# Kernel optimization log

Measured on AMD Instinct MI355X. Metric: run time of the kernel, lower is better.

Reference implementation:

```python
import jax, jax.numpy as jnp
import numpy as np
from jax import lax

D_MODEL = 1024
D_IN = 1024        # expand=1 -> d_inner = d_model
N_STATE = 16       # d_state
DT_RANK = 64       # ceil(d_model/16)
D_FFN = 4096
BATCH, SEQ = 2, 2048


def setup_inputs() -> dict:
    key = jax.random.key(0)
    ks = jax.random.split(key, 12)
    r = lambda i, shape, s=0.02: jax.random.normal(ks[i], shape, jnp.float32) * s
    ones = lambda n: jnp.ones((n,), jnp.float32)
    zeros = lambda n: jnp.zeros((n,), jnp.float32)
    # S4D-real init for A
    A_log = jnp.log(jnp.tile(jnp.arange(1, N_STATE + 1, dtype=jnp.float32), (D_IN, 1)))
    return {
        "src": jax.random.normal(ks[0], (BATCH, SEQ, D_MODEL), jnp.float32),
        "in_proj_w": r(1, (2 * D_IN, D_MODEL)),
        "conv_w": r(2, (D_IN, 2), 0.5),
        "conv_b": zeros(D_IN),
        "x_proj_w": r(3, (DT_RANK + 2 * N_STATE, D_IN)),
        "dt_proj_w": r(4, (D_IN, DT_RANK), 0.1),
        "dt_proj_b": r(5, (D_IN,), 0.1),
        "A_log": A_log,
        "Dp": ones(D_IN),
        "out_proj_w": r(6, (D_MODEL, D_IN)),
        "mnorm_g": ones(D_MODEL), "mnorm_b": zeros(D_MODEL),
        "n1_g": ones(D_MODEL), "n1_b": zeros(D_MODEL),
        "n2_g": ones(D_MODEL), "n2_b": zeros(D_MODEL),
        "n3_g": ones(D_MODEL), "n3_b": zeros(D_MODEL),
        "ffn_w1": r(7, (D_FFN, D_MODEL)),
        "ffn_w2": r(8, (D_MODEL, D_FFN)),
        "fe_w": r(9, (D_MODEL, D_MODEL)),
        "fe_b": zeros(D_MODEL),
    }


def _ln(x, g, b, eps=1e-5):
    m = x.mean(-1, keepdims=True)
    v = ((x - m) ** 2).mean(-1, keepdims=True)
    return (x - m) / jnp.sqrt(v + eps) * g + b


def _mamba(x, in_proj_w, conv_w, conv_b, x_proj_w, dt_proj_w, dt_proj_b,
           A_log, Dp, out_proj_w):
    B, L, _ = x.shape
    xz = x @ in_proj_w.T                       # (B,L,2*D_IN)
    x_in, z = jnp.split(xz, 2, axis=-1)
    # depthwise causal conv1d, kernel size 2: y[l] = w0*x[l-1] + w1*x[l] + b
    x_prev = jnp.pad(x_in, ((0, 0), (1, 0), (0, 0)))[:, :L]
    x_c = jax.nn.silu(x_prev * conv_w[:, 0] + x_in * conv_w[:, 1] + conv_b)
    x_dbl = x_c @ x_proj_w.T                   # (B,L,DT_RANK+2N)
    dt, Bm, Cm = jnp.split(x_dbl, [DT_RANK, DT_RANK + N_STATE], axis=-1)
    delta = jax.nn.softplus(dt @ dt_proj_w.T + dt_proj_b)   # (B,L,D_IN)
    A = -jnp.exp(A_log)                        # (D_IN,N)
    deltaA = jnp.exp(delta[..., None] * A)                   # (B,L,D_IN,N)
    dBu = delta[..., None] * Bm[:, :, None, :] * x_c[..., None]

    def step(h, t):
        dA_t, dBu_t, C_t = t                   # (B,D_IN,N),(B,D_IN,N),(B,N)
        h = dA_t * h + dBu_t
        y = jnp.einsum('bdn,bn->bd', h, C_t)
        return h, y

    h0 = jnp.zeros((B, D_IN, N_STATE), x.dtype)
    _, ys = lax.scan(step, h0,
                     (deltaA.transpose(1, 0, 2, 3),
                      dBu.transpose(1, 0, 2, 3),
                      Cm.transpose(1, 0, 2)))
    y = ys.transpose(1, 0, 2)                  # (B,L,D_IN)
    y = (y + x_c * Dp) * jax.nn.silu(z)
    return y @ out_proj_w.T


def reference(src, in_proj_w, conv_w, conv_b, x_proj_w, dt_proj_w, dt_proj_b,
              A_log, Dp, out_proj_w, mnorm_g, mnorm_b, n1_g, n1_b, n2_g, n2_b,
              n3_g, n3_b, ffn_w1, ffn_w2, fe_w, fe_b):
    # src1 = MambaBlock(norm1(src)); dropout = identity (eval)
    h = _mamba(_ln(src, n1_g, n1_b), in_proj_w, conv_w, conv_b, x_proj_w,
               dt_proj_w, dt_proj_b, A_log, Dp, out_proj_w)
    src = src + _ln(h, mnorm_g, mnorm_b)
    # FFN: Linear -> LeakyReLU(0.01) -> Linear (no bias)
    f = _ln(src, n2_g, n2_b) @ ffn_w1.T
    f = jnp.where(f >= 0, f, 0.01 * f) @ ffn_w2.T
    src = src + f
    src = src + (_ln(src, n3_g, n3_b) @ fe_w.T + fe_b)
    return src
```

## Files before the change

### kernel.cpp

```cpp
#include <hip/hip_runtime.h>
#include <hip/hip_bf16.h>
#include <cstddef>

#define L_SEQ   2048
#define NBATCH  2
#define NROWS   (NBATCH * L_SEQ)
#define NSTATE  16
#define CH      64
#define NCHUNK  (L_SEQ / CH)

typedef __bf16 bf16x8 __attribute__((ext_vector_type(8)));
typedef float  f32x4  __attribute__((ext_vector_type(4)));
typedef unsigned short u16x4 __attribute__((ext_vector_type(4)));
typedef unsigned short u16x8 __attribute__((ext_vector_type(8)));

static __device__ __forceinline__ unsigned short f2bf(float f) {
  unsigned int x = __builtin_bit_cast(unsigned int, f);
  x += 0x7fffu + ((x >> 16) & 1u);
  return (unsigned short)(x >> 16);
}
static __device__ __forceinline__ float bf2f(unsigned short u) {
  return __builtin_bit_cast(float, ((unsigned int)u) << 16);
}

#define GLDS(g, l) __builtin_amdgcn_global_load_lds( \
    (const __attribute__((address_space(1))) void*)(g), \
    (__attribute__((address_space(3))) void*)(l), 16, 0, 0)

#define DRAIN_VM() asm volatile("s_waitcnt vmcnt(0)" ::: "memory")

__global__ __launch_bounds__(256) void cvt_bf16_kernel(
    const float* __restrict__ in, unsigned short* __restrict__ out, int n4)
{
  const int i = blockIdx.x * 256 + threadIdx.x;
  if (i < n4) {
    const float4 v = reinterpret_cast<const float4*>(in)[i];
    u16x4 o;
    o[0] = f2bf(v.x); o[1] = f2bf(v.y); o[2] = f2bf(v.z); o[3] = f2bf(v.w);
    reinterpret_cast<u16x4*>(out)[i] = o;
  }
}

__global__ __launch_bounds__(256) void cvt_all_kernel(
    const float* __restrict__ ipw, const float* __restrict__ xpw,
    const float* __restrict__ dtw, const float* __restrict__ opw,
    const float* __restrict__ w1,  const float* __restrict__ w2,
    const float* __restrict__ few, float* __restrict__ zx,
    unsigned short* __restrict__ o_ipw, unsigned short* __restrict__ o_xpw,
    unsigned short* __restrict__ o_dtw, unsigned short* __restrict__ o_opw,
    unsigned short* __restrict__ o_w1,  unsigned short* __restrict__ o_w2,
    unsigned short* __restrict__ o_few,
    const float* __restrict__ lsrc, const float* __restrict__ lg,
    const float* __restrict__ lb, unsigned short* __restrict__ louth)
{
  __shared__ float sm[8];
  if (blockIdx.x >= 12832) {
    const int row = blockIdx.x - 12832;
    const int tid = threadIdx.x;
    const float4 v = reinterpret_cast<const float4*>(lsrc + (size_t)row * 1024)[tid];
    float s = v.x + v.y + v.z + v.w;
#pragma unroll
    for (int o = 32; o > 0; o >>= 1) s += __shfl_down(s, o, 64);
    if ((tid & 63) == 0) sm[tid >> 6] = s;
    __syncthreads();
    const float mean = (sm[0] + sm[1] + sm[2] + sm[3]) * (1.f / 1024.f);
    const float dx = v.x - mean, dy = v.y - mean, dz = v.z - mean, dw = v.w - mean;
    float q = dx * dx + dy * dy + dz * dz + dw * dw;
#pragma unroll
    for (int o = 32; o > 0; o >>= 1) q += __shfl_down(q, o, 64);
    __syncthreads();
    if ((tid & 63) == 0) sm[tid >> 6] = q;
    __syncthreads();
    const float var = (sm[0] + sm[1] + sm[2] + sm[3]) * (1.f / 1024.f);
    const float rstd = rsqrtf(var + 1e-5f);
    const float4 gv = reinterpret_cast<const float4*>(lg)[tid];
    const float4 bv = reinterpret_cast<const float4*>(lb)[tid];
    u16x4 ob;
    ob[0] = f2bf(dx * rstd * gv.x + bv.x);
    ob[1] = f2bf(dy * rstd * gv.y + bv.y);
    ob[2] = f2bf(dz * rstd * gv.z + bv.z);
    ob[3] = f2bf(dw * rstd * gv.w + bv.w);
    reinterpret_cast<u16x4*>(louth + (size_t)row * 1024)[tid] = ob;
    return;
  }
  int i = blockIdx.x * 256 + threadIdx.x;
  if (i < 98304) {
    reinterpret_cast<float4*>(zx)[i] = make_float4(0.f, 0.f, 0.f, 0.f);
    return;
  }
  i -= 98304;
  const float* src; unsigned short* dst;
  if (i < 524288)                 { src = ipw; dst = o_ipw; }
  else if ((i -= 524288) < 24576) { src = xpw; dst = o_xpw; }
  else if ((i -= 24576) < 16384)  { src = dtw; dst = o_dtw; }
  else if ((i -= 16384) < 262144) { src = opw; dst = o_opw; }
  else if ((i -= 262144) < 1048576){ src = w1; dst = o_w1; }
  else if ((i -= 1048576) < 1048576){ src = w2; dst = o_w2; }
  else if ((i -= 1048576) < 262144){ src = few; dst = o_few; }
  else return;
  const float4 v = reinterpret_cast<const float4*>(src)[i];
  u16x4 o;
  o[0] = f2bf(v.x); o[1] = f2bf(v.y); o[2] = f2bf(v.z); o[3] = f2bf(v.w);
  reinterpret_cast<u16x4*>(dst)[i] = o;
}

__global__ __launch_bounds__(256) void ln_kernel(
    const float* __restrict__ in, const float* __restrict__ g,
    const float* __restrict__ bta, const float* __restrict__ res,
    float* __restrict__ out, unsigned short* __restrict__ outb)
{
  const int row = blockIdx.x;
  const int tid = threadIdx.x;
  __shared__ float sm[8];
  const float4 v = reinterpret_cast<const float4*>(in + (size_t)row * 1024)[tid];
  float s = v.x + v.y + v.z + v.w;
#pragma unroll
  for (int o = 32; o > 0; o >>= 1) s += __shfl_down(s, o, 64);
  if ((tid & 63) == 0) sm[tid >> 6] = s;
  __syncthreads();
  const float mean = (sm[0] + sm[1] + sm[2] + sm[3]) * (1.f / 1024.f);
  const float dx = v.x - mean, dy = v.y - mean, dz = v.z - mean, dw = v.w - mean;
  float q = dx * dx + dy * dy + dz * dz + dw * dw;
#pragma unroll
  for (int o = 32; o > 0; o >>= 1) q += __shfl_down(q, o, 64);
  __syncthreads();
  if ((tid & 63) == 0) sm[tid >> 6] = q;
  __syncthreads();
  const float var = (sm[0] + sm[1] + sm[2] + sm[3]) * (1.f / 1024.f);
  const float rstd = rsqrtf(var + 1e-5f);
  const float4 gv = reinterpret_cast<const float4*>(g)[tid];
  const float4 bv = reinterpret_cast<const float4*>(bta)[tid];
  float4 o4;
  o4.x = dx * rstd * gv.x + bv.x;
  o4.y = dy * rstd * gv.y + bv.y;
  o4.z = dz * rstd * gv.z + bv.z;
  o4.w = dw * rstd * gv.w + bv.w;
  if (outb) {
    u16x4 ob;
    ob[0] = f2bf(o4.x); ob[1] = f2bf(o4.y); ob[2] = f2bf(o4.z); ob[3] = f2bf(o4.w);
    reinterpret_cast<u16x4*>(outb + (size_t)row * 1024)[tid] = ob;
  } else {
    if (res) {
      const float4 rv = reinterpret_cast<const float4*>(res + (size_t)row * 1024)[tid];
      o4.x += rv.x; o4.y += rv.y; o4.z += rv.z; o4.w += rv.w;
    }
    reinterpret_cast<float4*>(out + (size_t)row * 1024)[tid] = o4;
  }
}

__global__ __launch_bounds__(256) void ln2_kernel(
    const float* __restrict__ in, const float* __restrict__ g1,
    const float* __restrict__ b1, const float* __restrict__ res,
    const float* __restrict__ g2, const float* __restrict__ b2,
    float* __restrict__ out1, unsigned short* __restrict__ out2b)
{
  const int row = blockIdx.x;
  const int tid = threadIdx.x;
  __shared__ float sm[8];
  const float4 v = reinterpret_cast<const float4*>(in + (size_t)row * 1024)[tid];
  float s = v.x + v.y + v.z + v.w;
#pragma unroll
  for (int o = 32; o > 0; o >>= 1) s += __shfl_down(s, o, 64);
  if ((tid & 63) == 0) sm[tid >> 6] = s;
  __syncthreads();
  const float mean = (sm[0] + sm[1] + sm[2] + sm[3]) * (1.f / 1024.f);
  const float dx = v.x - mean, dy = v.y - mean, dz = v.z - mean, dw = v.w - mean;
  float q = dx * dx + dy * dy + dz * dz + dw * dw;
#pragma unroll
  for (int o = 32; o > 0; o >>= 1) q += __shfl_down(q, o, 64);
  __syncthreads();
  if ((tid & 63) == 0) sm[tid >> 6] = q;
  __syncthreads();
  const float var = (sm[0] + sm[1] + sm[2] + sm[3]) * (1.f / 1024.f);
  const float rstd = rsqrtf(var + 1e-5f);
  const float4 g1v = reinterpret_cast<const float4*>(g1)[tid];
  const float4 b1v = reinterpret_cast<const float4*>(b1)[tid];
  const float4 rv = reinterpret_cast<const float4*>(res + (size_t)row * 1024)[tid];
  float4 o4;
  o4.x = dx * rstd * g1v.x + b1v.x + rv.x;
  o4.y = dy * rstd * g1v.y + b1v.y + rv.y;
  o4.z = dz * rstd * g1v.z + b1v.z + rv.z;
  o4.w = dw * rstd * g1v.w + b1v.w + rv.w;
  reinterpret_cast<float4*>(out1 + (size_t)row * 1024)[tid] = o4;
  __syncthreads();
  float s2 = o4.x + o4.y + o4.z + o4.w;
#pragma unroll
  for (int o = 32; o > 0; o >>= 1) s2 += __shfl_down(s2, o, 64);
  if ((tid & 63) == 0) sm[tid >> 6] = s2;
  __syncthreads();
  const float mean2 = (sm[0] + sm[1] + sm[2] + sm[3]) * (1.f / 1024.f);
  const float ex = o4.x - mean2, ey = o4.y - mean2, ez = o4.z - mean2, ew = o4.w - mean2;
  float q2 = ex * ex + ey * ey + ez * ez + ew * ew;
#pragma unroll
  for (int o = 32; o > 0; o >>= 1) q2 += __shfl_down(q2, o, 64);
  __syncthreads();
  if ((tid & 63) == 0) sm[tid >> 6] = q2;
  __syncthreads();
  const float var2 = (sm[0] + sm[1] + sm[2] + sm[3]) * (1.f / 1024.f);
  const float rstd2 = rsqrtf(var2 + 1e-5f);
  const float4 g2v = reinterpret_cast<const float4*>(g2)[tid];
  const float4 b2v = reinterpret_cast<const float4*>(b2)[tid];
  u16x4 ob;
  ob[0] = f2bf(ex * rstd2 * g2v.x + b2v.x);
  ob[1] = f2bf(ey * rstd2 * g2v.y + b2v.y);
  ob[2] = f2bf(ez * rstd2 * g2v.z + b2v.z);
  ob[3] = f2bf(ew * rstd2 * g2v.w + b2v.w);
  reinterpret_cast<u16x4*>(out2b + (size_t)row * 1024)[tid] = ob;
}

__global__ __launch_bounds__(512) void gemm256_kernel(
    const unsigned short* __restrict__ A, int lda,
    const unsigned short* __restrict__ B, int ldb,
    void* __restrict__ Cv, int ldc,
    const float* __restrict__ bias, const float* __restrict__ res,
    int K, int act, int outbf, int gy)
{
  __shared__ __align__(16) unsigned char smem[131072];
  const int t = threadIdx.x;
  const int w = t >> 6, l = t & 63;

  const int q = gridDim.x >> 3;
  const int nid = (blockIdx.x & 7) * q + (blockIdx.x >> 3);
  const int bm = (nid / gy) * 256;
  const int bn = (nid % gy) * 256;

  const int wr = (w >> 2) * 128;
  const int wc = (w & 3) * 64;
  f32x4 acc[8][4] = {};

  const int srow = t >> 2;
  const int sk = (t & 3) * 8;
  const unsigned short* gA = A + (size_t)(bm + srow) * lda + sk;
  const unsigned short* gB = B + (size_t)(bn + srow) * ldb + sk;

  const int fr = l & 15;
  const int kb = (l >> 4) * 8;

#define SA7(s) (smem + (s) * 16384)
#define SB7(s) (smem + 65536 + (s) * 16384)

#define STAGE7(s, k0) do { \
    GLDS(gA + (k0), SA7(s) + w * 1024); \
    GLDS(gA + (k0) + (size_t)128 * lda, SA7(s) + 8192 + w * 1024); \
    GLDS(gB + (k0), SB7(s) + w * 1024); \
    GLDS(gB + (k0) + (size_t)128 * ldb, SB7(s) + 8192 + w * 1024); \
  } while (0)

#define COMPUTE7(s) do { \
    bf16x8 af[8], bfr[4]; \
    _Pragma("unroll") \
    for (int j = 0; j < 4; ++j) \
      bfr[j] = *reinterpret_cast<const bf16x8*>((const unsigned short*)SB7(s) + (wc + j * 16 + fr) * 32 + kb); \
    _Pragma("unroll") \
    for (int i = 0; i < 8; ++i) \
      af[i] = *reinterpret_cast<const bf16x8*>((const unsigned short*)SA7(s) + (wr + i * 16 + fr) * 32 + kb); \
    _Pragma("unroll") \
    for (int i = 0; i < 8; ++i) \
      _Pragma("unroll") \
      for (int j = 0; j < 4; ++j) \
        acc[i][j] = __builtin_amdgcn_mfma_f32_16x16x32_bf16(af[i], bfr[j], acc[i][j], 0, 0, 0); \
  } while (0)

  const int nt = K >> 5;
  STAGE7(0, 0);
  if (nt > 1) STAGE7(1, 32);
  if (nt > 2) STAGE7(2, 64);
  if (nt > 2)      asm volatile("s_waitcnt vmcnt(8)" ::: "memory");
  else if (nt > 1) asm volatile("s_waitcnt vmcnt(4)" ::: "memory");
  else             asm volatile("s_waitcnt vmcnt(0)" ::: "memory");
  __builtin_amdgcn_s_barrier();
  for (int kt = 0; kt < nt; ++kt) {
    const int s = kt & 3;
    __builtin_amdgcn_sched_barrier(0);
    if (kt + 3 < nt) STAGE7((kt + 3) & 3, (kt + 3) * 32);
    __builtin_amdgcn_sched_barrier(0);
    COMPUTE7(s);
    __builtin_amdgcn_sched_barrier(0);
    if (kt + 3 < nt)      asm volatile("s_waitcnt vmcnt(8)" ::: "memory");
    else if (kt + 2 < nt) asm volatile("s_waitcnt vmcnt(4)" ::: "memory");
    else if (kt + 1 < nt) asm volatile("s_waitcnt vmcnt(0)" ::: "memory");
    __builtin_amdgcn_s_barrier();
  }
#undef STAGE7
#undef COMPUTE7
#undef SA7
#undef SB7

  const int crow = (l >> 4) * 4;
  const int ccol = l & 15;
  float* Cf = (float*)Cv;
  unsigned short* Cb = (unsigned short*)Cv;
#pragma unroll
  for (int i = 0; i < 8; ++i) {
#pragma unroll
    for (int j = 0; j < 4; ++j) {
      const int n = bn + wc + j * 16 + ccol;
      const float bv = bias ? bias[n] : 0.f;
#pragma unroll
      for (int r = 0; r < 4; ++r) {
        const int m = bm + wr + i * 16 + crow + r;
        float v = acc[i][j][r] + bv;
        if (act == 1) v = (v > 20.f) ? v : __logf(1.f + __expf(v));
        else if (act == 2) v = (v >= 0.f) ? v : 0.01f * v;
        if (res) v += res[(size_t)m * ldc + n];
        if (outbf) Cb[(size_t)m * ldc + n] = f2bf(v);
        else       Cf[(size_t)m * ldc + n] = v;
      }
    }
  }
}

template<int BK>
__global__ __launch_bounds__(512) void gemm_ksplit_kernel(
    const unsigned short* __restrict__ A, int lda,
    const unsigned short* __restrict__ B, int ldb,
    void* __restrict__ Cv, int ldc,
    const float* __restrict__ bias, const float* __restrict__ res,
    int K, int act, int outbf, int gy)
{
  constexpr int ABYTES = 128 * BK * 2;
  constexpr int NISS = (BK == 32) ? 2 : 4;
  constexpr int RPI  = (BK == 32) ? 64 : 32;
  constexpr int NS   = BK / 32;
  __shared__ __align__(16) unsigned char smem[8 * ABYTES];
  const int tid = threadIdx.x;
  const int grp = tid >> 8;
  const int t = tid & 255;
  const int w = t >> 6, l = t & 63;

  const int q = gridDim.x >> 3;
  const int nid = (blockIdx.x & 7) * q + (blockIdx.x >> 3);
  const int bm = (nid / gy) * 128;
  const int bn = (nid % gy) * 128;

  const int K2 = K >> 1;
  const int koff = grp * K2;
  const int wr = (w >> 1) * 64, wc = (w & 1) * 64;
  f32x4 acc[4][4] = {};

  const int srow = (BK == 32) ? (t >> 2) : (t >> 3);
  const int sk   = (BK == 32) ? ((t & 3) * 8) : ((t & 7) * 8);
  const unsigned short* gA = A + (size_t)(bm + srow) * lda + koff + sk;
  const unsigned short* gB = B + (size_t)(bn + srow) * ldb + koff + sk;

  const int gbase = grp * 2 * ABYTES;
  const int fr = l & 15;
  const int kb = (l >> 4) * 8;

#define SAb(buf) (smem + gbase + (buf) * ABYTES)
#define SBb(buf) (smem + 4 * ABYTES + gbase + (buf) * ABYTES)

#define STAGEK(buf, k0) do { \
    _Pragma("unroll") \
    for (int ii = 0; ii < NISS; ++ii) { \
      GLDS(gA + (k0) + (size_t)ii * RPI * lda, SAb(buf) + ii * 4096 + w * 1024); \
      GLDS(gB + (k0) + (size_t)ii * RPI * ldb, SBb(buf) + ii * 4096 + w * 1024); \
    } \
  } while (0)

#define COMPUTEK(buf) do { \
    _Pragma("unroll") \
    for (int s = 0; s < NS; ++s) { \
      bf16x8 af[4], bfr[4]; \
      _Pragma("unroll") \
      for (int i = 0; i < 4; ++i) \
        af[i] = *reinterpret_cast<const bf16x8*>((const unsigned short*)SAb(buf) + (wr + i * 16 + fr) * BK + s * 32 + kb); \
      _Pragma("unroll") \
      for (int j = 0; j < 4; ++j) \
        bfr[j] = *reinterpret_cast<const bf16x8*>((const unsigned short*)SBb(buf) + (wc + j * 16 + fr) * BK + s * 32 + kb); \
      _Pragma("unroll") \
      for (int i = 0; i < 4; ++i) \
        _Pragma("unroll") \
        for (int j = 0; j < 4; ++j) \
          acc[i][j] = __builtin_amdgcn_mfma_f32_16x16x32_bf16(af[i], bfr[j], acc[i][j], 0, 0, 0); \
    } \
  } while (0)

  STAGEK(0, 0);
  DRAIN_VM();
  __syncthreads();
  int cur = 0;
  for (int k0 = BK; k0 < K2; k0 += BK) {
    __builtin_amdgcn_sched_barrier(0);
    STAGEK(cur ^ 1, k0);
    __builtin_amdgcn_sched_barrier(0);
    COMPUTEK(cur);
    DRAIN_VM();
    __syncthreads();
    cur ^= 1;
  }
  COMPUTEK(cur);
#undef STAGEK
#undef COMPUTEK
#undef SAb
#undef SBb

  __syncthreads();
  float* red = (float*)smem;
  if (grp) {
#pragma unroll
    for (int i = 0; i < 4; ++i)
#pragma unroll
      for (int j = 0; j < 4; ++j)
        *reinterpret_cast<f32x4*>(&red[(t << 6) + (i * 4 + j) * 4]) = acc[i][j];
  }
  __syncthreads();
  if (!grp) {
    const int crow = (l >> 4) * 4;
    const int ccol = l & 15;
    float* Cf = (float*)Cv;
    unsigned short* Cb = (unsigned short*)Cv;
#pragma unroll
    for (int i = 0; i < 4; ++i) {
#pragma unroll
      for (int j = 0; j < 4; ++j) {
        const f32x4 o = *reinterpret_cast<const f32x4*>(&red[(t << 6) + (i * 4 + j) * 4]);
        const int n = bn + wc + j * 16 + ccol;
        const float bv = bias ? bias[n] : 0.f;
#pragma unroll
        for (int r = 0; r < 4; ++r) {
          const int m = bm + wr + i * 16 + crow + r;
          float v = acc[i][j][r] + o[r] + bv;
          if (act == 1) v = (v > 20.f) ? v : __logf(1.f + __expf(v));
          else if (act == 2) v = (v >= 0.f) ? v : 0.01f * v;
          if (res) v += res[(size_t)m * ldc + n];
          if (outbf) Cb[(size_t)m * ldc + n] = f2bf(v);
          else       Cf[(size_t)m * ldc + n] = v;
        }
      }
    }
  }
}

__global__ __launch_bounds__(512) void gemm_ksplit_bn64_kernel(
    const unsigned short* __restrict__ A, int lda,
    const unsigned short* __restrict__ B, int ldb,
    void* __restrict__ Cv, int ldc,
    const float* __restrict__ bias, const float* __restrict__ res,
    int K, int act, int outbf, int gy)
{
  __shared__ __align__(16) unsigned char smem[49152];
  const int tid = threadIdx.x;
  const int grp = tid >> 8;
  const int t = tid & 255;
  const int w = t >> 6, l = t & 63;

  const int q = gridDim.x >> 3;
  const int nid = (blockIdx.x & 7) * q + (blockIdx.x >> 3);
  const int bm = (nid / gy) * 128;
  const int bn = (nid % gy) * 64;

  const int K2 = K >> 1;
  const int koff = grp * K2;
  const int wr = (w >> 1) * 64, wc = (w & 1) * 32;
  f32x4 acc[4][2] = {};

  const int srow = t >> 2;
  const int sk = (t & 3) * 8;
  const unsigned short* gA = A + (size_t)(bm + srow) * lda + koff + sk;
  const unsigned short* gB = B + (size_t)(bn + srow) * ldb + koff + sk;

  const int fr = l & 15;
  const int kb = (l >> 4) * 8;

#define SAn(buf) (smem + grp * 16384 + (buf) * 8192)
#define SBn(buf) (smem + 32768 + grp * 8192 + (buf) * 4096)

#define STAGEN(buf, k0) do { \
    GLDS(gA + (k0), SAn(buf) + w * 1024); \
    GLDS(gA + (k0) + (size_t)64 * lda, SAn(buf) + 4096 + w * 1024); \
    GLDS(gB + (k0), SBn(buf) + w * 1024); \
  } while (0)

#define COMPUTEN(buf) do { \
    bf16x8 af[4], bfr[2]; \
    _Pragma("unroll") \
    for (int i = 0; i < 4; ++i) \
      af[i] = *reinterpret_cast<const bf16x8*>((const unsigned short*)SAn(buf) + (wr + i * 16 + fr) * 32 + kb); \
    _Pragma("unroll") \
    for (int j = 0; j < 2; ++j) \
      bfr[j] = *reinterpret_cast<const bf16x8*>((const unsigned short*)SBn(buf) + (wc + j * 16 + fr) * 32 + kb); \
    _Pragma("unroll") \
    for (int i = 0; i < 4; ++i) \
      _Pragma("unroll") \
      for (int j = 0; j < 2; ++j) \
        acc[i][j] = __builtin_amdgcn_mfma_f32_16x16x32_bf16(af[i], bfr[j], acc[i][j], 0, 0, 0); \
  } while (0)

  STAGEN(0, 0);
  DRAIN_VM();
  __syncthreads();
  int cur = 0;
  for (int k0 = 32; k0 < K2; k0 += 32) {
    __builtin_amdgcn_sched_barrier(0);
    STAGEN(cur ^ 1, k0);
    __builtin_amdgcn_sched_barrier(0);
    COMPUTEN(cur);
    DRAIN_VM();
    __syncthreads();
    cur ^= 1;
  }
  COMPUTEN(cur);
#undef STAGEN
#undef COMPUTEN
#undef SAn
#undef SBn

  __syncthreads();
  float* red = (float*)smem;
  if (grp) {
#pragma unroll
    for (int i = 0; i < 4; ++i)
#pragma unroll
      for (int j = 0; j < 2; ++j)
        *reinterpret_cast<f32x4*>(&red[(t << 5) + (i * 2 + j) * 4]) = acc[i][j];
  }
  __syncthreads();
  if (!grp) {
    const int crow = (l >> 4) * 4;
    const int ccol = l & 15;
    float* Cf = (float*)Cv;
    unsigned short* Cb = (unsigned short*)Cv;
#pragma unroll
    for (int i = 0; i < 4; ++i) {
#pragma unroll
      for (int j = 0; j < 2; ++j) {
        const f32x4 o = *reinterpret_cast<const f32x4*>(&red[(t << 5) + (i * 2 + j) * 4]);
        const int n = bn + wc + j * 16 + ccol;
        const float bv = bias ? bias[n] : 0.f;
#pragma unroll
        for (int r = 0; r < 4; ++r) {
          const int m = bm + wr + i * 16 + crow + r;
          float v = acc[i][j][r] + o[r] + bv;
          if (act == 1) v = (v > 20.f) ? v : __logf(1.f + __expf(v));
          else if (act == 2) v = (v >= 0.f) ? v : 0.01f * v;
          if (res) v += res[(size_t)m * ldc + n];
          if (outbf) Cb[(size_t)m * ldc + n] = f2bf(v);
          else       Cf[(size_t)m * ldc + n] = v;
        }
      }
    }
  }
}

__global__ __launch_bounds__(512) void gemm_ksplit_ring_kernel(
    const unsigned short* __restrict__ A, int lda,
    const unsigned short* __restrict__ B, int ldb,
    void* __restrict__ Cv, int ldc,
    const float* __restrict__ bias, const float* __restrict__ res,
    int K, int act, int outbf, int gy)
{
  __shared__ __align__(16) unsigned char smem[131072];
  const int tid = threadIdx.x;
  const int grp = tid >> 8;
  const int t = tid & 255;
  const int w = t >> 6, l = t & 63;

  const int q = gridDim.x >> 3;
  const int nid = (blockIdx.x & 7) * q + (blockIdx.x >> 3);
  const int bm = (nid / gy) * 128;
  const int bn = (nid % gy) * 128;

  const int K2 = K >> 1;
  const int koff = grp * K2;
  const int wr = (w >> 1) * 64, wc = (w & 1) * 64;
  f32x4 acc[4][4] = {};

  const int srow = t >> 2;
  const int sk = (t & 3) * 8;
  const unsigned short* gA = A + (size_t)(bm + srow) * lda + koff + sk;
  const unsigned short* gB = B + (size_t)(bn + srow) * ldb + koff + sk;

  const int fr = l & 15;
  const int kb = (l >> 4) * 8;

#define SAr(s) (smem + grp * 32768 + (s) * 8192)
#define SBr(s) (smem + 65536 + grp * 32768 + (s) * 8192)

#define STAGER(s, k0) do { \
    GLDS(gA + (k0), SAr(s) + w * 1024); \
    GLDS(gA + (k0) + (size_t)64 * lda, SAr(s) + 4096 + w * 1024); \
    GLDS(gB + (k0), SBr(s) + w * 1024); \
    GLDS(gB + (k0) + (size_t)64 * ldb, SBr(s) + 4096 + w * 1024); \
  } while (0)

#define COMPUTER(s) do { \
    bf16x8 af[4], bfr[4]; \
    _Pragma("unroll") \
    for (int i = 0; i < 4; ++i) \
      af[i] = *reinterpret_cast<const bf16x8*>((const unsigned short*)SAr(s) + (wr + i * 16 + fr) * 32 + kb); \
    _Pragma("unroll") \
    for (int j = 0; j < 4; ++j) \
      bfr[j] = *reinterpret_cast<const bf16x8*>((const unsigned short*)SBr(s) + (wc + j * 16 + fr) * 32 + kb); \
    _Pragma("unroll") \
    for (int i = 0; i < 4; ++i) \
      _Pragma("unroll") \
      for (int j = 0; j < 4; ++j) \
        acc[i][j] = __builtin_amdgcn_mfma_f32_16x16x32_bf16(af[i], bfr[j], acc[i][j], 0, 0, 0); \
  } while (0)

  const int nt = K2 >> 5;
  STAGER(0, 0);
  if (nt > 1) STAGER(1, 32);
  if (nt > 2) STAGER(2, 64);
  if (nt > 2)      asm volatile("s_waitcnt vmcnt(8)" ::: "memory");
  else if (nt > 1) asm volatile("s_waitcnt vmcnt(4)" ::: "memory");
  else             asm volatile("s_waitcnt vmcnt(0)" ::: "memory");
  __builtin_amdgcn_s_barrier();
  for (int kt = 0; kt < nt; ++kt) {
    const int s = kt & 3;
    __builtin_amdgcn_sched_barrier(0);
    if (kt + 3 < nt) STAGER((kt + 3) & 3, (kt + 3) * 32);
    __builtin_amdgcn_sched_barrier(0);
    COMPUTER(s);
    __builtin_amdgcn_sched_barrier(0);
    if (kt + 3 < nt)      asm volatile("s_waitcnt vmcnt(8)" ::: "memory");
    else if (kt + 2 < nt) asm volatile("s_waitcnt vmcnt(4)" ::: "memory");
    else if (kt + 1 < nt) asm volatile("s_waitcnt vmcnt(0)" ::: "memory");
    __builtin_amdgcn_s_barrier();
  }
#undef STAGER
#undef COMPUTER
#undef SAr
#undef SBr

  __syncthreads();
  float* red = (float*)smem;
  if (grp) {
#pragma unroll
    for (int i = 0; i < 4; ++i)
#pragma unroll
      for (int j = 0; j < 4; ++j)
        *reinterpret_cast<f32x4*>(&red[(t << 6) + (i * 4 + j) * 4]) = acc[i][j];
  }
  __syncthreads();
  if (!grp) {
    const int crow = (l >> 4) * 4;
    const int ccol = l & 15;
    float* Cf = (float*)Cv;
    unsigned short* Cb = (unsigned short*)Cv;
#pragma unroll
    for (int i = 0; i < 4; ++i) {
#pragma unroll
      for (int j = 0; j < 4; ++j) {
        const f32x4 o = *reinterpret_cast<const f32x4*>(&red[(t << 6) + (i * 4 + j) * 4]);
        const int n = bn + wc + j * 16 + ccol;
        const float bv = bias ? bias[n] : 0.f;
#pragma unroll
        for (int r = 0; r < 4; ++r) {
          const int m = bm + wr + i * 16 + crow + r;
          float v = acc[i][j][r] + o[r] + bv;
          if (act == 1) v = (v > 20.f) ? v : __logf(1.f + __expf(v));
          else if (act == 2) v = (v >= 0.f) ? v : 0.01f * v;
          if (res) v += res[(size_t)m * ldc + n];
          if (outbf) Cb[(size_t)m * ldc + n] = f2bf(v);
          else       Cf[(size_t)m * ldc + n] = v;
        }
      }
    }
  }
}

__global__ __launch_bounds__(256) void xproj_kernel(
    const unsigned short* __restrict__ A, int lda,
    const unsigned short* __restrict__ B, int ldb,
    float* __restrict__ C)
{
  __shared__ unsigned short As[2][128 * 32];
  __shared__ unsigned short Bs[2][96 * 32];
  const int t = threadIdx.x;
  const int w = t >> 6, l = t & 63;
  const int bm = blockIdx.x * 128;
  const int kbase = blockIdx.y * 128;

  f32x4 acc[2][6] = {};

  const int srow = t >> 2;
  const int sk = (t & 3) * 8;
  const unsigned short* gA0 = A + (size_t)(bm + srow) * lda + kbase + sk;
  const unsigned short* gA1 = gA0 + (size_t)64 * lda;
  const unsigned short* gB0 = B + (size_t)srow * ldb + kbase + sk;
  const unsigned short* gB1 = gB0 + (size_t)64 * ldb;

  const int fr = l & 15;
  const int kb = (l >> 4) * 8;

#define STAGEX(buf, k0) do { \
    GLDS(gA0 + (k0), &As[buf][w * 512]); \
    GLDS(gA1 + (k0), &As[buf][2048 + w * 512]); \
    GLDS(gB0 + (k0), &Bs[buf][w * 512]); \
    if (w < 2) GLDS(gB1 + (k0), &Bs[buf][2048 + w * 512]); \
  } while (0)

#define COMPUTEX(buf) do { \
    bf16x8 af[2], bfr[6]; \
    _Pragma("unroll") \
    for (int i = 0; i < 2; ++i) \
      af[i] = *reinterpret_cast<const bf16x8*>(&As[buf][(w * 32 + i * 16 + fr) * 32 + kb]); \
    _Pragma("unroll") \
    for (int j = 0; j < 6; ++j) \
      bfr[j] = *reinterpret_cast<const bf16x8*>(&Bs[buf][(j * 16 + fr) * 32 + kb]); \
    _Pragma("unroll") \
    for (int i = 0; i < 2; ++i) \
      _Pragma("unroll") \
      for (int j = 0; j < 6; ++j) \
        acc[i][j] = __builtin_amdgcn_mfma_f32_16x16x32_bf16(af[i], bfr[j], acc[i][j], 0, 0, 0); \
  } while (0)

  STAGEX(0, 0);
  DRAIN_VM();
  __syncthreads();
  int cur = 0;
  for (int s = 1; s < 4; ++s) {
    __builtin_amdgcn_sched_barrier(0);
    STAGEX(cur ^ 1, s * 32);
    __builtin_amdgcn_sched_barrier(0);
    COMPUTEX(cur);
    DRAIN_VM();
    __syncthreads();
    cur ^= 1;
  }
  COMPUTEX(cur);
#undef STAGEX
#undef COMPUTEX

  const int crow = (l >> 4) * 4;
  const int ccol = l & 15;
#pragma unroll
  for (int i = 0; i < 2; ++i)
#pragma unroll
    for (int j = 0; j < 6; ++j)
#pragma unroll
      for (int r = 0; r < 4; ++r) {
        const int m = bm + w * 32 + i * 16 + crow + r;
        const int n = j * 16 + ccol;
        atomicAdd(&C[(size_t)m * 96 + n], acc[i][j][r]);
      }
}

__global__ __launch_bounds__(256) void conv_silu_kernel(
    const unsigned short* __restrict__ xz, const float* __restrict__ cw,
    const float* __restrict__ cb, unsigned short* __restrict__ xcb)
{
  const int i = blockIdx.x * 256 + threadIdx.x;
  const int row = i >> 7;
  const int dv = (i & 127) * 8;
  const int l = row & (L_SEQ - 1);
  const u16x8 cur = *reinterpret_cast<const u16x8*>(&xz[(size_t)row * 2048 + dv]);
  u16x8 prev = {};
  if (l != 0) prev = *reinterpret_cast<const u16x8*>(&xz[(size_t)(row - 1) * 2048 + dv]);
  float cwv[16], cbv[8];
#pragma unroll
  for (int qq = 0; qq < 4; ++qq)
    *reinterpret_cast<float4*>(&cwv[qq * 4]) = reinterpret_cast<const float4*>(cw + 2 * dv)[qq];
#pragma unroll
  for (int qq = 0; qq < 2; ++qq)
    *reinterpret_cast<float4*>(&cbv[qq * 4]) = reinterpret_cast<const float4*>(cb + dv)[qq];
  u16x8 o;
#pragma unroll
  for (int e = 0; e < 8; ++e) {
    const float v = bf2f(prev[e]) * cwv[2 * e] + bf2f(cur[e]) * cwv[2 * e + 1] + cbv[e];
    o[e] = f2bf(v / (1.f + __expf(-v)));
  }
  *reinterpret_cast<u16x8*>(&xcb[(size_t)row * 1024 + dv]) = o;
}

__global__ __launch_bounds__(256) void scan_pass1(
    const unsigned short* __restrict__ delta, const unsigned short* __restrict__ xc,
    const float* __restrict__ xdbl, const float* __restrict__ A_log,
    unsigned short* __restrict__ hfin, unsigned short* __restrict__ pcum)
{
  const int tid = threadIdx.x;
  const int db = blockIdx.x & 3;
  const int c = (blockIdx.x >> 2) & (NCHUNK - 1);
  const int b = blockIdx.x >> 7;
  const int d = db * 256 + tid;
  __shared__ float Bsh[CH][16];
  {
    const int lr = tid >> 2, q = tid & 3;
    const float* p = xdbl + ((size_t)(b * L_SEQ + c * CH + lr) * 96) + 64 + q * 4;
    *reinterpret_cast<float4*>(&Bsh[lr][q * 4]) = *reinterpret_cast<const float4*>(p);
  }
  float a[NSTATE];
#pragma unroll
  for (int n = 0; n < NSTATE; ++n) a[n] = -__expf(A_log[d * 16 + n]);
  __syncthreads();
  float h[NSTATE], P[NSTATE];
#pragma unroll
  for (int n = 0; n < NSTATE; ++n) { h[n] = 0.f; P[n] = 1.f; }
  const size_t rowbase = (size_t)(b * L_SEQ + c * CH);
  for (int s = 0; s < CH; ++s) {
    const size_t row = rowbase + s;
    const float dl = bf2f(delta[row * 1024 + d]);
    const float xcv = bf2f(xc[row * 1024 + d]);
#pragma unroll
    for (int n = 0; n < NSTATE; ++n) {
      const float dA = __expf(dl * a[n]);
      h[n] = h[n] * dA + (dl * Bsh[s][n]) * xcv;
      P[n] *= dA;
    }
  }
  const size_t base = ((size_t)((b * NCHUNK + c) * 1024 + d)) * 16;
  u16x8 h0, h1, p0, p1;
#pragma unroll
  for (int n = 0; n < 8; ++n) {
    h0[n] = f2bf(h[n]);     h1[n] = f2bf(h[n + 8]);
    p0[n] = f2bf(P[n]);     p1[n] = f2bf(P[n + 8]);
  }
  *reinterpret_cast<u16x8*>(hfin + base) = h0;
  *reinterpret_cast<u16x8*>(hfin + base + 8) = h1;
  *reinterpret_cast<u16x8*>(pcum + base) = p0;
  *reinterpret_cast<u16x8*>(pcum + base + 8) = p1;
}

__global__ __launch_bounds__(256) void scan_pass2(
    const unsigned short* __restrict__ hfin, const unsigned short* __restrict__ pcum,
    unsigned short* __restrict__ hstart)
{
  const int t = blockIdx.x * 256 + threadIdx.x;
  const int b = t >> 14;
  const int dn = t & 16383;
  const size_t base = (size_t)b * NCHUNK * 16384 + dn;
  float h = 0.f;
  for (int c = 0; c < NCHUNK; ++c) {
    const size_t idx = base + (size_t)c * 16384;
    hstart[idx] = f2bf(h);
    h = bf2f(pcum[idx]) * h + bf2f(hfin[idx]);
  }
}

__global__ __launch_bounds__(256) void scan_pass3(
    const unsigned short* __restrict__ delta, const unsigned short* __restrict__ xc,
    const float* __restrict__ xdbl, const float* __restrict__ A_log,
    const unsigned short* __restrict__ hstart, const float* __restrict__ Dp,
    const unsigned short* __restrict__ xz, unsigned short* __restrict__ yout)
{
  const int tid = threadIdx.x;
  const int db = blockIdx.x & 3;
  const int c = (blockIdx.x >> 2) & (NCHUNK - 1);
  const int b = blockIdx.x >> 7;
  const int d = db * 256 + tid;
  __shared__ float Bsh[CH][16];
  __shared__ float Csh[CH][16];
  {
    const int lr = tid >> 2, q = tid & 3;
    const float* p = xdbl + ((size_t)(b * L_SEQ + c * CH + lr) * 96);
    *reinterpret_cast<float4*>(&Bsh[lr][q * 4]) = *reinterpret_cast<const float4*>(p + 64 + q * 4);
    *reinterpret_cast<float4*>(&Csh[lr][q * 4]) = *reinterpret_cast<const float4*>(p + 80 + q * 4);
  }
  float a[NSTATE];
#pragma unroll
  for (int n = 0; n < NSTATE; ++n) a[n] = -__expf(A_log[d * 16 + n]);
  float h[NSTATE];
  {
    const size_t base = ((size_t)((b * NCHUNK + c) * 1024 + d)) * 16;
    const u16x8 v0 = *reinterpret_cast<const u16x8*>(hstart + base);
    const u16x8 v1 = *reinterpret_cast<const u16x8*>(hstart + base + 8);
#pragma unroll
    for (int n = 0; n < 8; ++n) { h[n] = bf2f(v0[n]); h[n + 8] = bf2f(v1[n]); }
  }
  const float dpv = Dp[d];
  __syncthreads();
  const size_t rowbase = (size_t)(b * L_SEQ + c * CH);
  for (int s = 0; s < CH; ++s) {
    const size_t row = rowbase + s;
    const float dl = bf2f(delta[row * 1024 + d]);
    const float xcv = bf2f(xc[row * 1024 + d]);
    float y = 0.f;
#pragma unroll
    for (int n = 0; n < NSTATE; ++n) {
      const float dA = __expf(dl * a[n]);
      h[n] = h[n] * dA + (dl * Bsh[s][n]) * xcv;
      y += h[n] * Csh[s][n];
    }
    const float z = bf2f(xz[row * 2048 + 1024 + d]);
    const float sil = z / (1.f + __expf(-z));
    yout[row * 1024 + d] = f2bf((y + xcv * dpv) * sil);
  }
}

extern "C" void kernel_launch(void* const* d_in, const int* in_sizes, int n_in,
                              void* d_out, int out_size, void* d_ws, size_t ws_size,
                              hipStream_t stream)
{
  (void)in_sizes; (void)n_in; (void)out_size; (void)ws_size;
  const float* src        = (const float*)d_in[0];
  const float* in_proj_w  = (const float*)d_in[1];
  const float* conv_w     = (const float*)d_in[2];
  const float* conv_b     = (const float*)d_in[3];
  const float* x_proj_w   = (const float*)d_in[4];
  const float* dt_proj_w  = (const float*)d_in[5];
  const float* dt_proj_b  = (const float*)d_in[6];
  const float* A_log      = (const float*)d_in[7];
  const float* Dp         = (const float*)d_in[8];
  const float* out_proj_w = (const float*)d_in[9];
  const float* mnorm_g    = (const float*)d_in[10];
  const float* mnorm_b    = (const float*)d_in[11];
  const float* n1_g       = (const float*)d_in[12];
  const float* n1_b       = (const float*)d_in[13];
  const float* n2_g       = (const float*)d_in[14];
  const float* n2_b       = (const float*)d_in[15];
  const float* n3_g       = (const float*)d_in[16];
  const float* n3_b       = (const float*)d_in[17];
  const float* ffn_w1     = (const float*)d_in[18];
  const float* ffn_w2     = (const float*)d_in[19];
  const float* fe_w       = (const float*)d_in[20];
  const float* fe_b       = (const float*)d_in[21];
  float* out = (float*)d_out;
  float* ws  = (float*)d_ws;

  unsigned short* xzb   = (unsigned short*)ws;
  unsigned short* xdblb = (unsigned short*)(ws + 4194304);
  unsigned short* dtwb  = (unsigned short*)(ws + 4390912);
  unsigned short* deltab= (unsigned short*)(ws + 4423680);
  float* xdbl  = ws + 12582912;
  float* s5    = ws + 17301504;
  float* src1  = ws + 21495808;
  unsigned short* hfin = (unsigned short*)(ws + 25690112);
  unsigned short* pcum = (unsigned short*)(ws + 26738688);
  unsigned short* hst  = (unsigned short*)(ws + 27787264);
  unsigned short* s1b  = (unsigned short*)(ws + 28835840);
  unsigned short* xcb  = (unsigned short*)(ws + 30932992);
  unsigned short* yb   = (unsigned short*)(ws + 33030144);
  unsigned short* f1b  = (unsigned short*)(ws + 35127296);
  unsigned short* ipwb = (unsigned short*)(ws + 43515904);
  unsigned short* xpwb = (unsigned short*)(ws + 44564480);
  unsigned short* opwb = (unsigned short*)(ws + 44613632);
  unsigned short* w1b  = (unsigned short*)(ws + 45137920);
  unsigned short* w2b  = (unsigned short*)(ws + 47235072);
  unsigned short* fewb = (unsigned short*)(ws + 49332224);

  const dim3 blk(256);
  const dim3 blk512(512);

  cvt_all_kernel<<<16928, blk, 0, stream>>>(
      in_proj_w, x_proj_w, dt_proj_w, out_proj_w, ffn_w1, ffn_w2, fe_w, xdbl,
      ipwb, xpwb, dtwb, opwb, w1b, w2b, fewb,
      src, n1_g, n1_b, s1b);

  gemm_ksplit_kernel<32><<<512, blk512, 0, stream>>>(s1b, 1024, ipwb, 1024, xzb, 2048,
                                                     nullptr, nullptr, 1024, 0, 1, 16);
  conv_silu_kernel<<<2048, blk, 0, stream>>>(xzb, conv_w, conv_b, xcb);
  xproj_kernel<<<dim3(32, 8), blk, 0, stream>>>(xcb, 1024, xpwb, 1024, xdbl);
  cvt_bf16_kernel<<<384, blk, 0, stream>>>(xdbl, xdblb, 98304);
  gemm_ksplit_kernel<32><<<256, blk512, 0, stream>>>(xdblb, 96, dtwb, 64, deltab, 1024,
                                                     dt_proj_b, nullptr, 64, 1, 1, 8);
  scan_pass1<<<256, blk, 0, stream>>>(deltab, xcb, xdbl, A_log, hfin, pcum);
  scan_pass2<<<128, blk, 0, stream>>>(hfin, pcum, hst);
  scan_pass3<<<256, blk, 0, stream>>>(deltab, xcb, xdbl, A_log, hst, Dp, xzb, yb);
  gemm_ksplit_bn64_kernel<<<512, blk512, 0, stream>>>(yb, 1024, opwb, 1024, s5, 1024,
                                                      nullptr, nullptr, 1024, 0, 0, 16);
  ln2_kernel<<<NROWS, blk, 0, stream>>>(s5, mnorm_g, mnorm_b, src,
                                        n2_g, n2_b, src1, s1b);
  gemm256_kernel<<<256, blk512, 0, stream>>>(s1b, 1024, w1b, 1024, f1b, 4096,
                                             nullptr, nullptr, 1024, 2, 1, 16);
  gemm_ksplit_ring_kernel<<<256, blk512, 0, stream>>>(f1b, 4096, w2b, 4096, s5, 1024,
                                                      nullptr, src1, 4096, 0, 0, 8);
  ln_kernel<<<NROWS, blk, 0, stream>>>(s5, n3_g, n3_b, nullptr, nullptr, s1b);
  gemm_ksplit_bn64_kernel<<<512, blk512, 0, stream>>>(s1b, 1024, fewb, 1024, out, 1024,
                                                      fe_b, s5, 1024, 0, 0, 16);
}
```

Before: 368.3 us.

## Split FFN down-projection GEMM K dimension four ways with 1024-thread blocks

Replaces the two-way intra-block K-split ring-pipelined GEMM for the FFN second projection with a four-way K-split using 1024-thread blocks. Each 256-thread group now processes a quarter of K with a double-buffered stage instead of a 4-deep ring, and partial sums are combined through a two-level shared-memory tree reduction. The aim is more waves per CU to hide memory latency on the long K=4096 reduction. In exchange, pipeline depth drops to two buffers with full vmcnt drains each step, register pressure rises under the 1024-thread launch bound, and the reduction adds extra barriers.

```diff
diff --git a/kernel.cpp b/kernel.cpp
--- a/kernel.cpp
+++ b/kernel.cpp
@@ -543,7 +543,7 @@
   }
 }
 
-__global__ __launch_bounds__(512) void gemm_ksplit_ring_kernel(
+__global__ __launch_bounds__(1024) void gemm_ksplit4_kernel(
     const unsigned short* __restrict__ A, int lda,
     const unsigned short* __restrict__ B, int ldb,
     void* __restrict__ Cv, int ldc,
@@ -561,8 +561,8 @@
   const int bm = (nid / gy) * 128;
   const int bn = (nid % gy) * 128;
 
-  const int K2 = K >> 1;
-  const int koff = grp * K2;
+  const int K4 = K >> 2;
+  const int koff = grp * K4;
   const int wr = (w >> 1) * 64, wc = (w & 1) * 64;
   f32x4 acc[4][4] = {};
 
@@ -574,24 +574,24 @@
   const int fr = l & 15;
   const int kb = (l >> 4) * 8;
 
-#define SAr(s) (smem + grp * 32768 + (s) * 8192)
-#define SBr(s) (smem + 65536 + grp * 32768 + (s) * 8192)
-
-#define STAGER(s, k0) do { \
-    GLDS(gA + (k0), SAr(s) + w * 1024); \
-    GLDS(gA + (k0) + (size_t)64 * lda, SAr(s) + 4096 + w * 1024); \
-    GLDS(gB + (k0), SBr(s) + w * 1024); \
-    GLDS(gB + (k0) + (size_t)64 * ldb, SBr(s) + 4096 + w * 1024); \
+#define SA4(buf) (smem + grp * 16384 + (buf) * 8192)
+#define SB4(buf) (smem + 65536 + grp * 16384 + (buf) * 8192)
+
+#define STAGE4(buf, k0) do { \
+    GLDS(gA + (k0), SA4(buf) + w * 1024); \
+    GLDS(gA + (k0) + (size_t)64 * lda, SA4(buf) + 4096 + w * 1024); \
+    GLDS(gB + (k0), SB4(buf) + w * 1024); \
+    GLDS(gB + (k0) + (size_t)64 * ldb, SB4(buf) + 4096 + w * 1024); \
   } while (0)
 
-#define COMPUTER(s) do { \
+#define COMPUTE4(buf) do { \
     bf16x8 af[4], bfr[4]; \
     _Pragma("unroll") \
     for (int i = 0; i < 4; ++i) \
-      af[i] = *reinterpret_cast<const bf16x8*>((const unsigned short*)SAr(s) + (wr + i * 16 + fr) * 32 + kb); \
+      af[i] = *reinterpret_cast<const bf16x8*>((const unsigned short*)SA4(buf) + (wr + i * 16 + fr) * 32 + kb); \
     _Pragma("unroll") \
     for (int j = 0; j < 4; ++j) \
-      bfr[j] = *reinterpret_cast<const bf16x8*>((const unsigned short*)SBr(s) + (wc + j * 16 + fr) * 32 + kb); \
+      bfr[j] = *reinterpret_cast<const bf16x8*>((const unsigned short*)SB4(buf) + (wc + j * 16 + fr) * 32 + kb); \
     _Pragma("unroll") \
     for (int i = 0; i < 4; ++i) \
       _Pragma("unroll") \
@@ -599,42 +599,65 @@
         acc[i][j] = __builtin_amdgcn_mfma_f32_16x16x32_bf16(af[i], bfr[j], acc[i][j], 0, 0, 0); \
   } while (0)
 
-  const int nt = K2 >> 5;
-  STAGER(0, 0);
-  if (nt > 1) STAGER(1, 32);
-  if (nt > 2) STAGER(2, 64);
-  if (nt > 2)      asm volatile("s_waitcnt vmcnt(8)" ::: "memory");
-  else if (nt > 1) asm volatile("s_waitcnt vmcnt(4)" ::: "memory");
-  else             asm volatile("s_waitcnt vmcnt(0)" ::: "memory");
-  __builtin_amdgcn_s_barrier();
-  for (int kt = 0; kt < nt; ++kt) {
-    const int s = kt & 3;
-    __builtin_amdgcn_sched_barrier(0);
-    if (kt + 3 < nt) STAGER((kt + 3) & 3, (kt + 3) * 32);
-    __builtin_amdgcn_sched_barrier(0);
-    COMPUTER(s);
-    __builtin_amdgcn_sched_barrier(0);
-    if (kt + 3 < nt)      asm volatile("s_waitcnt vmcnt(8)" ::: "memory");
-    else if (kt + 2 < nt) asm volatile("s_waitcnt vmcnt(4)" ::: "memory");
-    else if (kt + 1 < nt) asm volatile("s_waitcnt vmcnt(0)" ::: "memory");
-    __builtin_amdgcn_s_barrier();
-  }
-#undef STAGER
-#undef COMPUTER
-#undef SAr
-#undef SBr
-
-  __syncthreads();
-  float* red = (float*)smem;
-  if (grp) {
+  STAGE4(0, 0);
+  DRAIN_VM();
+  __syncthreads();
+  int cur = 0;
+  for (int k0 = 32; k0 < K4; k0 += 32) {
+    __builtin_amdgcn_sched_barrier(0);
+    STAGE4(cur ^ 1, k0);
+    __builtin_amdgcn_sched_barrier(0);
+    COMPUTE4(cur);
+    DRAIN_VM();
+    __syncthreads();
+    cur ^= 1;
+  }
+  COMPUTE4(cur);
+#undef STAGE4
+#undef COMPUTE4
+#undef SA4
+#undef SB4
+
+  __syncthreads();
+  float* red1 = (float*)smem;
+  float* red3 = (float*)(smem + 65536);
+  if (grp == 1) {
 #pragma unroll
     for (int i = 0; i < 4; ++i)
 #pragma unroll
       for (int j = 0; j < 4; ++j)
-        *reinterpret_cast<f32x4*>(&red[(t << 6) + (i * 4 + j) * 4]) = acc[i][j];
-  }
-  __syncthreads();
-  if (!grp) {
+        *reinterpret_cast<f32x4*>(&red1[(t << 6) + (i * 4 + j) * 4]) = acc[i][j];
+  } else if (grp == 3) {
+#pragma unroll
+    for (int i = 0; i < 4; ++i)
+#pragma unroll
+      for (int j = 0; j < 4; ++j)
+        *reinterpret_cast<f32x4*>(&red3[(t << 6) + (i * 4 + j) * 4]) = acc[i][j];
+  }
+  __syncthreads();
+  if (grp == 0) {
+#pragma unroll
+    for (int i = 0; i < 4; ++i)
+#pragma unroll
+      for (int j = 0; j < 4; ++j)
+        acc[i][j] += *reinterpret_cast<const f32x4*>(&red1[(t << 6) + (i * 4 + j) * 4]);
+  } else if (grp == 2) {
+#pragma unroll
+    for (int i = 0; i < 4; ++i)
+#pragma unroll
+      for (int j = 0; j < 4; ++j)
+        acc[i][j] += *reinterpret_cast<const f32x4*>(&red3[(t << 6) + (i * 4 + j) * 4]);
+  }
+  __syncthreads();
+  if (grp == 2) {
+#pragma unroll
+    for (int i = 0; i < 4; ++i)
+#pragma unroll
+      for (int j = 0; j < 4; ++j)
+        *reinterpret_cast<f32x4*>(&red1[(t << 6) + (i * 4 + j) * 4]) = acc[i][j];
+  }
+  __syncthreads();
+  if (grp == 0) {
     const int crow = (l >> 4) * 4;
     const int ccol = l & 15;
     float* Cf = (float*)Cv;
@@ -643,7 +666,7 @@
     for (int i = 0; i < 4; ++i) {
 #pragma unroll
       for (int j = 0; j < 4; ++j) {
-        const f32x4 o = *reinterpret_cast<const f32x4*>(&red[(t << 6) + (i * 4 + j) * 4]);
+        const f32x4 o = *reinterpret_cast<const f32x4*>(&red1[(t << 6) + (i * 4 + j) * 4]);
         const int n = bn + wc + j * 16 + ccol;
         const float bv = bias ? bias[n] : 0.f;
 #pragma unroll
@@ -932,6 +955,7 @@
 
   const dim3 blk(256);
   const dim3 blk512(512);
+  const dim3 blk1024(1024);
 
   cvt_all_kernel<<<16928, blk, 0, stream>>>(
       in_proj_w, x_proj_w, dt_proj_w, out_proj_w, ffn_w1, ffn_w2, fe_w, xdbl,
@@ -954,8 +978,8 @@
                                         n2_g, n2_b, src1, s1b);
   gemm256_kernel<<<256, blk512, 0, stream>>>(s1b, 1024, w1b, 1024, f1b, 4096,
                                              nullptr, nullptr, 1024, 2, 1, 16);
-  gemm_ksplit_ring_kernel<<<256, blk512, 0, stream>>>(f1b, 4096, w2b, 4096, s5, 1024,
-                                                      nullptr, src1, 4096, 0, 0, 8);
+  gemm_ksplit4_kernel<<<256, blk1024, 0, stream>>>(f1b, 4096, w2b, 4096, s5, 1024,
+                                                   nullptr, src1, 4096, 0, 0, 8);
   ln_kernel<<<NROWS, blk, 0, stream>>>(s5, n3_g, n3_b, nullptr, nullptr, s1b);
   gemm_ksplit_bn64_kernel<<<512, blk512, 0, stream>>>(s1b, 1024, fewb, 1024, out, 1024,
                                                       fe_b, s5, 1024, 0, 0, 16);
```

Measured after the change: 378.9 us. 1.03x slower.
